# Performance work log

Measured on AMD Instinct MI355X. Metric: run time of the kernel, lower is better.

Reference implementation:

```python
import jax, jax.numpy as jnp
import numpy as np

B, S, I, C, P = 64, 14, 32, 10, 4   # batch, spatial, in-caps/pos, classes, pose size
ROUTINGS = 3
EPS = 1e-9


def setup_inputs() -> dict:
    key = jax.random.key(0)
    k1, k2, k3, k4, k5 = jax.random.split(key, 5)
    return {
        "inputs_pose": jax.random.normal(k1, (B, S, S, I, P, P), jnp.float32),
        "inputs_activation": jax.random.uniform(k2, (B, S, S, I), jnp.float32),
        "w": jax.random.normal(k3, (1, I, C, P, P), jnp.float32),
        "beta_v": jax.random.normal(k4, (1, C), jnp.float32) * 0.1,
        "beta_a": jax.random.normal(k5, (1, C), jnp.float32) * 0.1,
    }


def _em_routing(votes, i_act, beta_v, beta_a, routings):
    # votes: [B, N, C, 16], i_act: [B, N]
    Bn, N, Cc, D = votes.shape
    rr = jnp.full((Bn, N, Cc, 1), 1.0 / Cc, votes.dtype)  # uniform init assignments
    bv = beta_v.reshape(1, 1, Cc, 1)
    ba = beta_a.reshape(1, 1, Cc, 1)
    it_min, it_max = 1.0, min(float(routings), 3.0)  # inverse-temperature schedule
    o_mean = o_act = None
    for it in range(routings):
        inv_temp = it_min + (it_max - it_min) * it / max(1.0, routings - 1.0)
        # --- M step ---
        rr_p = rr * i_act[:, :, None, None]                        # [B,N,C,1]
        rr_sum = jnp.sum(rr_p, axis=1, keepdims=True)              # [B,1,C,1]
        o_mean = jnp.sum(rr_p * votes, axis=1, keepdims=True) / rr_sum   # [B,1,C,16]
        o_var = jnp.sum(rr_p * jnp.square(votes - o_mean), axis=1, keepdims=True) / rr_sum
        o_stdv = jnp.sqrt(o_var)                                   # [B,1,C,16]
        cost = jnp.sum((bv + jnp.log(o_stdv + EPS)) * rr_sum, axis=-1, keepdims=True)  # [B,1,C,1]
        o_act = jax.nn.sigmoid(inv_temp * (ba - cost))             # [B,1,C,1]
        # --- E step (skipped on last iteration) ---
        if it < routings - 1:
            logp = (-jnp.sum(jnp.square(votes - o_mean) / (2.0 * jnp.square(o_stdv) + EPS),
                             axis=-1, keepdims=True)
                    - jnp.sum(jnp.log(o_stdv + EPS), axis=-1, keepdims=True))  # [B,N,C,1]
            zz = jnp.log(o_act + EPS) + logp
            rr = jax.nn.softmax(zz, axis=2)
    return o_mean[:, 0], o_act[:, 0, :, 0]  # [B,C,16], [B,C]


def reference(inputs_pose, inputs_activation, w, beta_v, beta_a):
    # mat_transform: votes[b,h,w,i,c] = pose[b,h,w,i] @ W[i,c]   (4x4 matmuls)
    votes = jnp.einsum('bhwipq,icqr->bhwicpr', inputs_pose, w[0])
    votes = votes.reshape(B, S, S, I, C, P * P)
    # coordinate addition: scaled (row+0.5)/S onto pose element 0, col onto element 1
    coord = (jnp.arange(S, dtype=votes.dtype) + 0.5) / S
    votes = votes.at[..., 0].add(coord[None, :, None, None, None])
    votes = votes.at[..., 1].add(coord[None, None, :, None, None])
    votes = votes.reshape(B, S * S * I, C, P * P)
    acts = inputs_activation.reshape(B, S * S * I)
    o_mean, o_act = _em_routing(votes, acts, beta_v, beta_a, ROUTINGS)
    pose = o_mean.reshape(B, C, P, P)
    return pose, o_act
```

## Files before the change

kernel.cpp:

```cpp
#include <hip/hip_runtime.h>
#include <math.h>

#define Bsz 64
#define Ssz 14
#define Isz 32
#define Csz 10
#define Psz 4
#define Dsz 16
#define Nsz (Ssz*Ssz*Isz)
#define EPSF 1e-9f

#define NCH 8
#define CHUNK 784

__global__ __launch_bounds__(640) void m_partial_kernel(
    const float* __restrict__ pose,
    const float* __restrict__ act,
    const float* __restrict__ w,
    const float* __restrict__ rr_p,
    float* __restrict__ partials,
    int uniform)
{
    const int b = blockIdx.x;
    const int chunk = blockIdx.y;
    const int tid = threadIdx.x;
    const int wave = tid >> 6;
    const int lane = tid & 63;

    __shared__ float Wm[Csz][Isz*17];

    for (int t = tid; t < Csz*Isz*Dsz; t += 640) {
        int c = t >> 9;
        int rem = t & 511;
        int i = rem >> 4, q = rem & 15;
        Wm[c][i*17 + q] = w[(i*Csz + c)*Dsz + q];
    }
    __syncthreads();

    const int c = wave;
    float s0 = 0.f;
    float s1[Dsz], s2[Dsz];
#pragma unroll
    for (int d = 0; d < Dsz; ++d) { s1[d] = 0.f; s2[d] = 0.f; }

    const float* poseb = pose + (size_t)b * Nsz * Dsz;
    const float* actb  = act  + (size_t)b * Nsz;
    const float* rrb   = rr_p + ((size_t)b * Csz + c) * Nsz;
    const float* Wc    = &Wm[c][0];

    const int n_end = chunk*CHUNK + CHUNK;
    for (int n = chunk*CHUNK + lane; n < n_end; n += 64) {
        const float4* pp = reinterpret_cast<const float4*>(poseb + (size_t)n * Dsz);
        float4 a0 = pp[0], a1 = pp[1], a2 = pp[2], a3 = pp[3];
        float p[16] = {a0.x,a0.y,a0.z,a0.w, a1.x,a1.y,a1.z,a1.w,
                       a2.x,a2.y,a2.z,a2.w, a3.x,a3.y,a3.z,a3.w};
        int i  = n & (Isz-1);
        int hw = n >> 5;
        int wcol = hw % Ssz, hrow = hw / Ssz;
        float wgt = uniform ? (actb[n] * (1.0f/Csz)) : rrb[n];

        const float* Wi = &Wc[i*17];
        float v[16];
#pragma unroll
        for (int pr = 0; pr < 4; ++pr) {
#pragma unroll
            for (int r = 0; r < 4; ++r) {
                v[pr*4+r] = p[pr*4+0]*Wi[0*4+r] + p[pr*4+1]*Wi[1*4+r]
                          + p[pr*4+2]*Wi[2*4+r] + p[pr*4+3]*Wi[3*4+r];
            }
        }
        v[0] += (hrow + 0.5f) * (1.0f/Ssz);
        v[1] += (wcol + 0.5f) * (1.0f/Ssz);

        s0 += wgt;
#pragma unroll
        for (int d = 0; d < Dsz; ++d) {
            float wv = wgt * v[d];
            s1[d] += wv;
            s2[d] += wv * v[d];
        }
    }

#pragma unroll
    for (int m = 32; m >= 1; m >>= 1) {
        s0 += __shfl_xor(s0, m);
#pragma unroll
        for (int d = 0; d < Dsz; ++d) {
            s1[d] += __shfl_xor(s1[d], m);
            s2[d] += __shfl_xor(s2[d], m);
        }
    }
    if (lane == 0) {
        float* pt = partials + ((size_t)(b*Csz + c)*NCH + chunk)*33;
        pt[0] = s0;
#pragma unroll
        for (int d = 0; d < Dsz; ++d) { pt[1+d] = s1[d]; pt[17+d] = s2[d]; }
    }
}

__global__ __launch_bounds__(64) void m_finalize_kernel(
    const float* __restrict__ partials,
    const float* __restrict__ beta_v,
    const float* __restrict__ beta_a,
    float* __restrict__ params,
    float* __restrict__ out,
    float inv_temp, int final_it)
{
    const int bc = blockIdx.x * 64 + threadIdx.x;
    if (bc >= Bsz*Csz) return;
    const int c = bc % Csz;

    float S[33];
#pragma unroll
    for (int j = 0; j < 33; ++j) S[j] = 0.f;
    const float* pb = partials + (size_t)bc * NCH * 33;
    for (int ch = 0; ch < NCH; ++ch)
#pragma unroll
        for (int j = 0; j < 33; ++j) S[j] += pb[ch*33 + j];

    float S0 = S[0];
    float rS0 = 1.f / S0;
    float sumlog = 0.f;
    float mean[16], invd[16];
#pragma unroll
    for (int d = 0; d < Dsz; ++d) {
        float S1 = S[1+d], S2 = S[17+d];
        float mn  = S1 * rS0;
        float var = fmaxf(S2 * rS0 - mn*mn, 0.f);
        float stdv = sqrtf(var);
        sumlog += __logf(stdv + EPSF);
        mean[d] = mn;
        invd[d] = 1.f / (2.f*var + EPSF);
    }
    float cost = S0 * (16.f * beta_v[c] + sumlog);
    float oact = 1.f / (1.f + __expf(-inv_temp * (beta_a[c] - cost)));

    float* prm = params + (size_t)bc * 33;
#pragma unroll
    for (int d = 0; d < Dsz; ++d) { prm[d] = mean[d]; prm[16+d] = invd[d]; }
    prm[32] = __logf(oact + EPSF) - sumlog;

    if (final_it) {
        float* om = out + (size_t)bc * Dsz;
#pragma unroll
        for (int d = 0; d < Dsz; ++d) om[d] = mean[d];
        out[Bsz*Csz*Dsz + bc] = oact;
    }
}

__global__ __launch_bounds__(256) void e_step_kernel(
    const float* __restrict__ pose,
    const float* __restrict__ act,
    const float* __restrict__ w,
    const float* __restrict__ params,
    float* __restrict__ rr_p)
{
    const int b = blockIdx.y;
    const int tid = threadIdx.x;
    const int n = blockIdx.x * 256 + tid;

    __shared__ float Wl[Isz*161];
    __shared__ float prm[Csz*33];

    for (int t = tid; t < Isz*Csz*Dsz; t += 256) {
        int i = t / (Csz*Dsz);
        int rest = t - i*(Csz*Dsz);
        Wl[i*161 + rest] = w[t];
    }
    for (int t = tid; t < Csz*33; t += 256)
        prm[t] = params[(size_t)b*Csz*33 + t];
    __syncthreads();

    if (n >= Nsz) return;

    const float4* pp = reinterpret_cast<const float4*>(pose + ((size_t)b * Nsz + n) * Dsz);
    float4 a0 = pp[0], a1 = pp[1], a2 = pp[2], a3 = pp[3];
    float p[16] = {a0.x,a0.y,a0.z,a0.w, a1.x,a1.y,a1.z,a1.w,
                   a2.x,a2.y,a2.z,a2.w, a3.x,a3.y,a3.z,a3.w};
    float a = act[(size_t)b*Nsz + n];
    const int i = n & (Isz-1);
    const int hw = n >> 5;
    const int wcol = hw % Ssz, hrow = hw / Ssz;
    const float ch = (hrow + 0.5f) * (1.0f/Ssz);
    const float cw = (wcol + 0.5f) * (1.0f/Ssz);

    float zz[Csz];
#pragma unroll
    for (int c = 0; c < Csz; ++c) {
        const float* Wi = &Wl[i*161 + c*16];
        const float* pc = &prm[c*33];
        float quad = 0.f;
#pragma unroll
        for (int pr = 0; pr < 4; ++pr) {
#pragma unroll
            for (int r = 0; r < 4; ++r) {
                float v = p[pr*4+0]*Wi[0*4+r] + p[pr*4+1]*Wi[1*4+r]
                        + p[pr*4+2]*Wi[2*4+r] + p[pr*4+3]*Wi[3*4+r];
                const int d = pr*4 + r;
                if (d == 0) v += ch;
                if (d == 1) v += cw;
                float dv = v - pc[d];
                quad += dv * dv * pc[16+d];
            }
        }
        zz[c] = pc[32] - quad;
    }

    float zmax = zz[0];
#pragma unroll
    for (int c = 1; c < Csz; ++c) zmax = fmaxf(zmax, zz[c]);
    float zsum = 0.f;
#pragma unroll
    for (int c = 0; c < Csz; ++c) { zz[c] = __expf(zz[c] - zmax); zsum += zz[c]; }
    const float sc = __fdividef(a, zsum);
#pragma unroll
    for (int c = 0; c < Csz; ++c)
        rr_p[((size_t)b*Csz + c)*Nsz + n] = zz[c] * sc;
}

extern "C" void kernel_launch(void* const* d_in, const int* in_sizes, int n_in,
                              void* d_out, int out_size, void* d_ws, size_t ws_size,
                              hipStream_t stream)
{
    const float* pose = (const float*)d_in[0];
    const float* act  = (const float*)d_in[1];
    const float* w    = (const float*)d_in[2];
    const float* bv   = (const float*)d_in[3];
    const float* ba   = (const float*)d_in[4];
    float* out = (float*)d_out;

    float* rr_p     = (float*)d_ws;
    float* partials = rr_p + (size_t)Bsz*Csz*Nsz;
    float* params   = partials + (size_t)Bsz*Csz*NCH*33;

    dim3 mgrid(Bsz, NCH);
    dim3 egrid((Nsz + 255)/256, Bsz);
    dim3 fgrid((Bsz*Csz + 63)/64);

    m_partial_kernel<<<mgrid, 640, 0, stream>>>(pose, act, w, rr_p, partials, 1);
    m_finalize_kernel<<<fgrid, 64, 0, stream>>>(partials, bv, ba, params, out, 1.0f, 0);
    e_step_kernel<<<egrid, 256, 0, stream>>>(pose, act, w, params, rr_p);
    m_partial_kernel<<<mgrid, 640, 0, stream>>>(pose, act, w, rr_p, partials, 0);
    m_finalize_kernel<<<fgrid, 64, 0, stream>>>(partials, bv, ba, params, out, 2.0f, 0);
    e_step_kernel<<<egrid, 256, 0, stream>>>(pose, act, w, params, rr_p);
    m_partial_kernel<<<mgrid, 640, 0, stream>>>(pose, act, w, rr_p, partials, 0);
    m_finalize_kernel<<<fgrid, 64, 0, stream>>>(partials, bv, ba, params, out, 3.0f, 1);
}
```

Baseline: 232.4 us.

## Fuse finalize, E-step and M-step partials into one kernel per routing iteration

Each routing iteration now runs as a single kernel. Every block reduces the previous partial sums into Gaussian parameters in shared memory, computes the softmax assignments for its 640-element chunk into shared memory, and accumulates new weighted moments. This removes the global rr_p buffer write/read round-trip and cuts the launch count from eight to four. In exchange, every block redundantly recomputes the parameter finalize and computes the votes twice per chunk, and the chunk size and count change to 640 and 10.

```diff
diff --git a/kernel.cpp b/kernel.cpp
--- a/kernel.cpp
+++ b/kernel.cpp
@@ -5,79 +5,71 @@
 #define Ssz 14
 #define Isz 32
 #define Csz 10
-#define Psz 4
 #define Dsz 16
 #define Nsz (Ssz*Ssz*Isz)
 #define EPSF 1e-9f
 
-#define NCH 8
-#define CHUNK 784
-
-__global__ __launch_bounds__(640) void m_partial_kernel(
+#define CH  640
+#define NCH 10
+
+__device__ __forceinline__ void compute_vote(const float* __restrict__ p,
+                                             const float* __restrict__ Wi,
+                                             float chh, float cww, float* v)
+{
+#pragma unroll
+    for (int pr = 0; pr < 4; ++pr)
+#pragma unroll
+        for (int r = 0; r < 4; ++r)
+            v[pr*4+r] = p[pr*4+0]*Wi[0*4+r] + p[pr*4+1]*Wi[1*4+r]
+                      + p[pr*4+2]*Wi[2*4+r] + p[pr*4+3]*Wi[3*4+r];
+    v[0] += chh;
+    v[1] += cww;
+}
+
+__global__ __launch_bounds__(640) void m0_kernel(
     const float* __restrict__ pose,
     const float* __restrict__ act,
     const float* __restrict__ w,
-    const float* __restrict__ rr_p,
-    float* __restrict__ partials,
-    int uniform)
-{
-    const int b = blockIdx.x;
-    const int chunk = blockIdx.y;
-    const int tid = threadIdx.x;
-    const int wave = tid >> 6;
-    const int lane = tid & 63;
+    float* __restrict__ partials)
+{
+    const int b = blockIdx.x, chunk = blockIdx.y;
+    const int tid = threadIdx.x, c = tid >> 6, lane = tid & 63;
 
     __shared__ float Wm[Csz][Isz*17];
 
     for (int t = tid; t < Csz*Isz*Dsz; t += 640) {
-        int c = t >> 9;
-        int rem = t & 511;
-        int i = rem >> 4, q = rem & 15;
-        Wm[c][i*17 + q] = w[(i*Csz + c)*Dsz + q];
-    }
-    __syncthreads();
-
-    const int c = wave;
-    float s0 = 0.f;
-    float s1[Dsz], s2[Dsz];
+        int cc = t >> 9, rem = t & 511, i = rem >> 4, q = rem & 15;
+        Wm[cc][i*17 + q] = w[(i*Csz + cc)*Dsz + q];
+    }
+    __syncthreads();
+
+    float s0 = 0.f, s1[Dsz], s2[Dsz];
 #pragma unroll
     for (int d = 0; d < Dsz; ++d) { s1[d] = 0.f; s2[d] = 0.f; }
 
     const float* poseb = pose + (size_t)b * Nsz * Dsz;
     const float* actb  = act  + (size_t)b * Nsz;
-    const float* rrb   = rr_p + ((size_t)b * Csz + c) * Nsz;
-    const float* Wc    = &Wm[c][0];
-
-    const int n_end = chunk*CHUNK + CHUNK;
-    for (int n = chunk*CHUNK + lane; n < n_end; n += 64) {
-        const float4* pp = reinterpret_cast<const float4*>(poseb + (size_t)n * Dsz);
-        float4 a0 = pp[0], a1 = pp[1], a2 = pp[2], a3 = pp[3];
-        float p[16] = {a0.x,a0.y,a0.z,a0.w, a1.x,a1.y,a1.z,a1.w,
-                       a2.x,a2.y,a2.z,a2.w, a3.x,a3.y,a3.z,a3.w};
-        int i  = n & (Isz-1);
-        int hw = n >> 5;
-        int wcol = hw % Ssz, hrow = hw / Ssz;
-        float wgt = uniform ? (actb[n] * (1.0f/Csz)) : rrb[n];
-
-        const float* Wi = &Wc[i*17];
-        float v[16];
-#pragma unroll
-        for (int pr = 0; pr < 4; ++pr) {
-#pragma unroll
-            for (int r = 0; r < 4; ++r) {
-                v[pr*4+r] = p[pr*4+0]*Wi[0*4+r] + p[pr*4+1]*Wi[1*4+r]
-                          + p[pr*4+2]*Wi[2*4+r] + p[pr*4+3]*Wi[3*4+r];
+    const int base = chunk * CH;
+
+    for (int nl = lane; nl < CH; nl += 64) {
+        const int n = base + nl;
+        if (n < Nsz) {
+            const float4* pp = reinterpret_cast<const float4*>(poseb + (size_t)n * Dsz);
+            float4 a0 = pp[0], a1 = pp[1], a2 = pp[2], a3 = pp[3];
+            float p[16] = {a0.x,a0.y,a0.z,a0.w, a1.x,a1.y,a1.z,a1.w,
+                           a2.x,a2.y,a2.z,a2.w, a3.x,a3.y,a3.z,a3.w};
+            int i = n & 31, hw = n >> 5;
+            int wc = hw % Ssz, hr = hw / Ssz;
+            float wgt = actb[n] * (1.0f/Csz);
+            float v[16];
+            compute_vote(p, &Wm[c][i*17], (hr+0.5f)*(1.0f/Ssz), (wc+0.5f)*(1.0f/Ssz), v);
+            s0 += wgt;
+#pragma unroll
+            for (int d = 0; d < Dsz; ++d) {
+                float wv = wgt * v[d];
+                s1[d] += wv;
+                s2[d] += wv * v[d];
             }
-        }
-        v[0] += (hrow + 0.5f) * (1.0f/Ssz);
-        v[1] += (wcol + 0.5f) * (1.0f/Ssz);
-
-        s0 += wgt;
-#pragma unroll
-        for (int d = 0; d < Dsz; ++d) {
-            float wv = wgt * v[d];
-            s1[d] += wv;
-            s2[d] += wv * v[d];
         }
     }
 
@@ -98,13 +90,149 @@
     }
 }
 
-__global__ __launch_bounds__(64) void m_finalize_kernel(
+__global__ __launch_bounds__(640) void em_kernel(
+    const float* __restrict__ pose,
+    const float* __restrict__ act,
+    const float* __restrict__ w,
+    const float* __restrict__ beta_v,
+    const float* __restrict__ beta_a,
+    const float* __restrict__ part_in,
+    float* __restrict__ part_out,
+    float inv_temp_prev)
+{
+    const int b = blockIdx.x, chunk = blockIdx.y;
+    const int tid = threadIdx.x, wv = tid >> 6, lane = tid & 63;
+
+    __shared__ float Wm[Csz][Isz*17];
+    __shared__ float rr[Csz][CH];
+    __shared__ float prm[Csz][33];
+    __shared__ float Sv[Csz][33];
+    __shared__ float lg[Csz][16];
+
+    for (int t = tid; t < Csz*Isz*Dsz; t += 640) {
+        int cc = t >> 9, rem = t & 511, i = rem >> 4, q = rem & 15;
+        Wm[cc][i*17 + q] = w[(i*Csz + cc)*Dsz + q];
+    }
+    if (tid < Csz*33) {
+        int c = tid / 33, j = tid - c*33;
+        const float* pp = part_in + ((size_t)(b*Csz + c)*NCH)*33 + j;
+        float s = 0.f;
+        for (int ch2 = 0; ch2 < NCH; ++ch2) s += pp[ch2*33];
+        Sv[c][j] = s;
+    }
+    __syncthreads();
+    if (tid < Csz*Dsz) {
+        int c = tid >> 4, d = tid & 15;
+        float S0 = Sv[c][0];
+        float mn  = Sv[c][1+d] / S0;
+        float var = fmaxf(Sv[c][17+d] / S0 - mn*mn, 0.f);
+        float stdv = sqrtf(var);
+        prm[c][d]    = mn;
+        prm[c][16+d] = 1.f / (2.f*var + EPSF);
+        lg[c][d]     = __logf(stdv + EPSF);
+    }
+    __syncthreads();
+    if (tid < Csz) {
+        int c = tid;
+        float sumlog = 0.f;
+#pragma unroll
+        for (int d = 0; d < Dsz; ++d) sumlog += lg[c][d];
+        float cost = Sv[c][0] * (16.f * beta_v[c] + sumlog);
+        float oact = 1.f / (1.f + __expf(-inv_temp_prev * (beta_a[c] - cost)));
+        prm[c][32] = __logf(oact + EPSF) - sumlog;
+    }
+    __syncthreads();
+
+    const int base = chunk * CH;
+    const float* poseb = pose + (size_t)b * Nsz * Dsz;
+    {
+        const int n = base + tid;
+        if (n < Nsz) {
+            const float4* pp = reinterpret_cast<const float4*>(poseb + (size_t)n * Dsz);
+            float4 a0 = pp[0], a1 = pp[1], a2 = pp[2], a3 = pp[3];
+            float p[16] = {a0.x,a0.y,a0.z,a0.w, a1.x,a1.y,a1.z,a1.w,
+                           a2.x,a2.y,a2.z,a2.w, a3.x,a3.y,a3.z,a3.w};
+            int i = n & 31, hw = n >> 5;
+            int wc = hw % Ssz, hr = hw / Ssz;
+            float chh = (hr+0.5f)*(1.0f/Ssz), cww = (wc+0.5f)*(1.0f/Ssz);
+            float a = act[(size_t)b*Nsz + n];
+
+            float zz[Csz];
+#pragma unroll
+            for (int c = 0; c < Csz; ++c) {
+                float v[16];
+                compute_vote(p, &Wm[c][i*17], chh, cww, v);
+                float quad = 0.f;
+#pragma unroll
+                for (int d = 0; d < Dsz; ++d) {
+                    float dv = v[d] - prm[c][d];
+                    quad += dv * dv * prm[c][16+d];
+                }
+                zz[c] = prm[c][32] - quad;
+            }
+            float zmax = zz[0];
+#pragma unroll
+            for (int c = 1; c < Csz; ++c) zmax = fmaxf(zmax, zz[c]);
+            float zsum = 0.f;
+#pragma unroll
+            for (int c = 0; c < Csz; ++c) { zz[c] = __expf(zz[c] - zmax); zsum += zz[c]; }
+            float sc = __fdividef(a, zsum);
+#pragma unroll
+            for (int c = 0; c < Csz; ++c) rr[c][tid] = zz[c] * sc;
+        }
+    }
+    __syncthreads();
+
+    const int c = wv;
+    float s0 = 0.f, s1[Dsz], s2[Dsz];
+#pragma unroll
+    for (int d = 0; d < Dsz; ++d) { s1[d] = 0.f; s2[d] = 0.f; }
+
+    for (int nl = lane; nl < CH; nl += 64) {
+        const int n = base + nl;
+        if (n < Nsz) {
+            const float4* pp = reinterpret_cast<const float4*>(poseb + (size_t)n * Dsz);
+            float4 a0 = pp[0], a1 = pp[1], a2 = pp[2], a3 = pp[3];
+            float p[16] = {a0.x,a0.y,a0.z,a0.w, a1.x,a1.y,a1.z,a1.w,
+                           a2.x,a2.y,a2.z,a2.w, a3.x,a3.y,a3.z,a3.w};
+            int i = n & 31, hw = n >> 5;
+            int wc = hw % Ssz, hr = hw / Ssz;
+            float wgt = rr[c][nl];
+            float v[16];
+            compute_vote(p, &Wm[c][i*17], (hr+0.5f)*(1.0f/Ssz), (wc+0.5f)*(1.0f/Ssz), v);
+            s0 += wgt;
+#pragma unroll
+            for (int d = 0; d < Dsz; ++d) {
+                float wvv = wgt * v[d];
+                s1[d] += wvv;
+                s2[d] += wvv * v[d];
+            }
+        }
+    }
+
+#pragma unroll
+    for (int m = 32; m >= 1; m >>= 1) {
+        s0 += __shfl_xor(s0, m);
+#pragma unroll
+        for (int d = 0; d < Dsz; ++d) {
+            s1[d] += __shfl_xor(s1[d], m);
+            s2[d] += __shfl_xor(s2[d], m);
+        }
+    }
+    if (lane == 0) {
+        float* pt = part_out + ((size_t)(b*Csz + c)*NCH + chunk)*33;
+        pt[0] = s0;
+#pragma unroll
+        for (int d = 0; d < Dsz; ++d) { pt[1+d] = s1[d]; pt[17+d] = s2[d]; }
+    }
+}
+
+__global__ __launch_bounds__(64) void fin_kernel(
     const float* __restrict__ partials,
     const float* __restrict__ beta_v,
     const float* __restrict__ beta_a,
-    float* __restrict__ params,
     float* __restrict__ out,
-    float inv_temp, int final_it)
+    float inv_temp)
 {
     const int bc = blockIdx.x * 64 + threadIdx.x;
     if (bc >= Bsz*Csz) return;
@@ -114,108 +242,23 @@
 #pragma unroll
     for (int j = 0; j < 33; ++j) S[j] = 0.f;
     const float* pb = partials + (size_t)bc * NCH * 33;
-    for (int ch = 0; ch < NCH; ++ch)
-#pragma unroll
-        for (int j = 0; j < 33; ++j) S[j] += pb[ch*33 + j];
-
-    float S0 = S[0];
-    float rS0 = 1.f / S0;
+    for (int ch2 = 0; ch2 < NCH; ++ch2)
+#pragma unroll
+        for (int j = 0; j < 33; ++j) S[j] += pb[ch2*33 + j];
+
+    float S0 = S[0], rS0 = 1.f / S0;
     float sumlog = 0.f;
-    float mean[16], invd[16];
+    float* om = out + (size_t)bc * Dsz;
 #pragma unroll
     for (int d = 0; d < Dsz; ++d) {
-        float S1 = S[1+d], S2 = S[17+d];
-        float mn  = S1 * rS0;
-        float var = fmaxf(S2 * rS0 - mn*mn, 0.f);
-        float stdv = sqrtf(var);
-        sumlog += __logf(stdv + EPSF);
-        mean[d] = mn;
-        invd[d] = 1.f / (2.f*var + EPSF);
+        float mn  = S[1+d] * rS0;
+        float var = fmaxf(S[17+d] * rS0 - mn*mn, 0.f);
+        sumlog += __logf(sqrtf(var) + EPSF);
+        om[d] = mn;
     }
     float cost = S0 * (16.f * beta_v[c] + sumlog);
     float oact = 1.f / (1.f + __expf(-inv_temp * (beta_a[c] - cost)));
-
-    float* prm = params + (size_t)bc * 33;
-#pragma unroll
-    for (int d = 0; d < Dsz; ++d) { prm[d] = mean[d]; prm[16+d] = invd[d]; }
-    prm[32] = __logf(oact + EPSF) - sumlog;
-
-    if (final_it) {
-        float* om = out + (size_t)bc * Dsz;
-#pragma unroll
-        for (int d = 0; d < Dsz; ++d) om[d] = mean[d];
-        out[Bsz*Csz*Dsz + bc] = oact;
-    }
-}
-
-__global__ __launch_bounds__(256) void e_step_kernel(
-    const float* __restrict__ pose,
-    const float* __restrict__ act,
-    const float* __restrict__ w,
-    const float* __restrict__ params,
-    float* __restrict__ rr_p)
-{
-    const int b = blockIdx.y;
-    const int tid = threadIdx.x;
-    const int n = blockIdx.x * 256 + tid;
-
-    __shared__ float Wl[Isz*161];
-    __shared__ float prm[Csz*33];
-
-    for (int t = tid; t < Isz*Csz*Dsz; t += 256) {
-        int i = t / (Csz*Dsz);
-        int rest = t - i*(Csz*Dsz);
-        Wl[i*161 + rest] = w[t];
-    }
-    for (int t = tid; t < Csz*33; t += 256)
-        prm[t] = params[(size_t)b*Csz*33 + t];
-    __syncthreads();
-
-    if (n >= Nsz) return;
-
-    const float4* pp = reinterpret_cast<const float4*>(pose + ((size_t)b * Nsz + n) * Dsz);
-    float4 a0 = pp[0], a1 = pp[1], a2 = pp[2], a3 = pp[3];
-    float p[16] = {a0.x,a0.y,a0.z,a0.w, a1.x,a1.y,a1.z,a1.w,
-                   a2.x,a2.y,a2.z,a2.w, a3.x,a3.y,a3.z,a3.w};
-    float a = act[(size_t)b*Nsz + n];
-    const int i = n & (Isz-1);
-    const int hw = n >> 5;
-    const int wcol = hw % Ssz, hrow = hw / Ssz;
-    const float ch = (hrow + 0.5f) * (1.0f/Ssz);
-    const float cw = (wcol + 0.5f) * (1.0f/Ssz);
-
-    float zz[Csz];
-#pragma unroll
-    for (int c = 0; c < Csz; ++c) {
-        const float* Wi = &Wl[i*161 + c*16];
-        const float* pc = &prm[c*33];
-        float quad = 0.f;
-#pragma unroll
-        for (int pr = 0; pr < 4; ++pr) {
-#pragma unroll
-            for (int r = 0; r < 4; ++r) {
-                float v = p[pr*4+0]*Wi[0*4+r] + p[pr*4+1]*Wi[1*4+r]
-                        + p[pr*4+2]*Wi[2*4+r] + p[pr*4+3]*Wi[3*4+r];
-                const int d = pr*4 + r;
-                if (d == 0) v += ch;
-                if (d == 1) v += cw;
-                float dv = v - pc[d];
-                quad += dv * dv * pc[16+d];
-            }
-        }
-        zz[c] = pc[32] - quad;
-    }
-
-    float zmax = zz[0];
-#pragma unroll
-    for (int c = 1; c < Csz; ++c) zmax = fmaxf(zmax, zz[c]);
-    float zsum = 0.f;
-#pragma unroll
-    for (int c = 0; c < Csz; ++c) { zz[c] = __expf(zz[c] - zmax); zsum += zz[c]; }
-    const float sc = __fdividef(a, zsum);
-#pragma unroll
-    for (int c = 0; c < Csz; ++c)
-        rr_p[((size_t)b*Csz + c)*Nsz + n] = zz[c] * sc;
+    out[Bsz*Csz*Dsz + bc] = oact;
 }
 
 extern "C" void kernel_launch(void* const* d_in, const int* in_sizes, int n_in,
@@ -229,20 +272,13 @@
     const float* ba   = (const float*)d_in[4];
     float* out = (float*)d_out;
 
-    float* rr_p     = (float*)d_ws;
-    float* partials = rr_p + (size_t)Bsz*Csz*Nsz;
-    float* params   = partials + (size_t)Bsz*Csz*NCH*33;
-
-    dim3 mgrid(Bsz, NCH);
-    dim3 egrid((Nsz + 255)/256, Bsz);
-    dim3 fgrid((Bsz*Csz + 63)/64);
-
-    m_partial_kernel<<<mgrid, 640, 0, stream>>>(pose, act, w, rr_p, partials, 1);
-    m_finalize_kernel<<<fgrid, 64, 0, stream>>>(partials, bv, ba, params, out, 1.0f, 0);
-    e_step_kernel<<<egrid, 256, 0, stream>>>(pose, act, w, params, rr_p);
-    m_partial_kernel<<<mgrid, 640, 0, stream>>>(pose, act, w, rr_p, partials, 0);
-    m_finalize_kernel<<<fgrid, 64, 0, stream>>>(partials, bv, ba, params, out, 2.0f, 0);
-    e_step_kernel<<<egrid, 256, 0, stream>>>(pose, act, w, params, rr_p);
-    m_partial_kernel<<<mgrid, 640, 0, stream>>>(pose, act, w, rr_p, partials, 0);
-    m_finalize_kernel<<<fgrid, 64, 0, stream>>>(partials, bv, ba, params, out, 3.0f, 1);
-}
+    float* partA = (float*)d_ws;
+    float* partB = partA + (size_t)Bsz*Csz*NCH*33;
+
+    dim3 grid(Bsz, NCH);
+
+    m0_kernel<<<grid, CH, 0, stream>>>(pose, act, w, partA);
+    em_kernel<<<grid, CH, 0, stream>>>(pose, act, w, bv, ba, partA, partB, 1.0f);
+    em_kernel<<<grid, CH, 0, stream>>>(pose, act, w, bv, ba, partB, partA, 2.0f);
+    fin_kernel<<<(Bsz*Csz + 63)/64, 64, 0, stream>>>(partA, bv, ba, out, 3.0f);
+}
```

Measured after the change: 226.2 us. 2.7% less time.
